# Performance work log

Measured on AMD Instinct MI355X. Metric: run time of the kernel, lower is better.

## Reference

```python
import jax, jax.numpy as jnp
import numpy as np

CTX_WIN = 3  # config.ctx_win_size


def setup_inputs() -> dict:
    key = jax.random.key(0)
    k1, k2, k3 = jax.random.split(key, 3)
    bsz, seq_len, h1, A = 32, 2048, 128, 8
    batch_docIn = jax.random.normal(k1, (bsz, seq_len, h1), dtype=jnp.float32)
    mask = jnp.ones((bsz, seq_len), dtype=bool)
    # params initialized uniform(-0.01, 0.01) as in the torch module
    aspEmbed_weight = jax.random.uniform(k2, (A, CTX_WIN * h1), minval=-0.01, maxval=0.01, dtype=jnp.float32)
    aspProj = jax.random.uniform(k3, (A, h1, h1), minval=-0.01, maxval=0.01, dtype=jnp.float32)
    return {"batch_docIn": batch_docIn, "mask": mask,
            "aspEmbed_weight": aspEmbed_weight, "aspProj": aspProj}


def reference(batch_docIn, mask, aspEmbed_weight, aspProj):
    b, s, h = batch_docIn.shape
    A = aspProj.shape[0]
    win = CTX_WIN
    pad = (win - 1) // 2

    # all aspects at once: [b, A, s, h]
    proj = jnp.einsum('bsd,adh->bash', batch_docIn, aspProj)
    padded = jnp.pad(proj, ((0, 0), (0, 0), (pad, pad), (0, 0)))

    embedR = aspEmbed_weight.reshape(A, h, win)
    # scores[b,a,s] = sum_{d,w} window[b,a,s,d,w] * embedR[a,d,w]
    # computed as a sum over the (small, fixed) window offsets to avoid
    scores = sum(jnp.einsum('bash,ah->bas', padded[:, :, w:w + s, :], embedR[:, :, w])
                 for w in range(win))

    # mask (bool [b,s]) -> masked_fill(~mask, -inf); softmax over seq dim
    scores = jnp.where(mask[:, None, :], scores, -jnp.inf)
    attn = jax.nn.softmax(scores, axis=-1)  # [b, A, s]

    # weighted sum over sequence: [b, A, h]
    rep = jnp.einsum('bash,bas->bah', proj, attn)

    # torch returns attn as [b, A, s] (after transpose/cat) and rep [b, A, h]
    return attn, rep
```

## Files before the change

### kernel.cpp

```cpp
#include <hip/hip_runtime.h>
#include <math.h>

#define BB 32
#define SS 2048
#define HH 128
#define AA 8

typedef _Float16 h2 __attribute__((ext_vector_type(2)));
typedef _Float16 h8 __attribute__((ext_vector_type(8)));
typedef _Float16 f16x8 __attribute__((ext_vector_type(8)));
typedef float f32x4 __attribute__((ext_vector_type(4)));


__global__ __launch_bounds__(128) void prep_kernel(const float* __restrict__ embed,
                                                   const float* __restrict__ proj,
                                                   uint4* __restrict__ bfrag) {
    __shared__ float ua[HH][3];
    int a = blockIdx.x;
    int d = threadIdx.x;
    const float* P = proj + ((size_t)a * HH + d) * HH;
    const float* E = embed + a * (3 * HH);
    float a0 = 0.f, a1 = 0.f, a2 = 0.f;
    for (int h = 0; h < HH; ++h) {
        float x = P[h];
        a0 += x * E[h * 3 + 0];
        a1 += x * E[h * 3 + 1];
        a2 += x * E[h * 3 + 2];
    }
    ua[d][0] = a0; ua[d][1] = a1; ua[d][2] = a2;
    __syncthreads();

    for (int i = d; i < 96; i += 128) {
        int kk = i >> 3, e = i & 7;
        f16x8 v = {0, 0, 0, 0, 0, 0, 0, 0};
        int lane;
        if (e < 4) {
            int q = e;
            lane = q * 16 + a;
            #pragma unroll
            for (int j = 0; j < 8; ++j) {
                int k = kk * 32 + q * 8 + j;
                int w = k >> 7, dd = k & 127;
                v[j] = (_Float16)ua[dd][w];
            }
        } else {
            lane = (e - 4) * 16 + a + 8;
        }
        bfrag[kk * 64 + lane] = __builtin_bit_cast(uint4, v);
    }
}

__global__ __launch_bounds__(256, 4) void tile_kernel(const float* __restrict__ doc,
                                                      const int* __restrict__ mask,
                                                      const uint4* __restrict__ bfrag,
                                                      float* __restrict__ E,
                                                      float* __restrict__ Zpart,
                                                      float* __restrict__ pools) {
    __shared__ __align__(16) unsigned char smraw[21312];
    h2*    dt    = (h2*)smraw;
    float* etile = (float*)(smraw + 19008);
    float* zred  = (float*)(smraw + 19008 + 2048);

    int t = threadIdx.x;
    int lane = t & 63, wave = t >> 6;
    int tile = blockIdx.x;
    int b = blockIdx.y;
    int s0 = tile * 64;

    for (int idx = t; idx < 66 * 16; idx += 256) {
        int row = idx >> 4, c = idx & 15;
        int srow = s0 - 1 + row;
        h8 hv = {0, 0, 0, 0, 0, 0, 0, 0};
        if (srow >= 0 && srow < SS) {
            const float4* src = (const float4*)(doc + ((size_t)b * SS + srow) * HH + c * 8);
            float4 v0 = src[0], v1 = src[1];
            hv[0] = (_Float16)v0.x; hv[1] = (_Float16)v0.y;
            hv[2] = (_Float16)v0.z; hv[3] = (_Float16)v0.w;
            hv[4] = (_Float16)v1.x; hv[5] = (_Float16)v1.y;
            hv[6] = (_Float16)v1.z; hv[7] = (_Float16)v1.w;
        }
        *(h8*)(dt + row * 72 + c * 4) = hv;
    }

    f16x8 bf[12];
    #pragma unroll
    for (int kk = 0; kk < 12; ++kk)
        bf[kk] = __builtin_bit_cast(f16x8, bfrag[kk * 64 + lane]);
    __syncthreads();

    f32x4 acc = {0.f, 0.f, 0.f, 0.f};
    #pragma unroll
    for (int kk = 0; kk < 12; ++kk) {
        int w = kk >> 2;
        int row = wave * 16 + (lane & 15) + w;
        int colh2 = (kk & 3) * 16 + (lane >> 4) * 4;
        f16x8 af = *(const f16x8*)(dt + row * 72 + colh2);
        acc = __builtin_amdgcn_mfma_f32_16x16x32_f16(af, bf[kk], acc, 0, 0, 0);
    }

    const int* mrow = mask + (size_t)b * SS + s0;
    {
        int a = lane & 15;
        int rbase = wave * 16 + (lane >> 4) * 4;
        if (a < 8) {
            float4 ev;
            float* evp = (float*)&ev;
            #pragma unroll
            for (int jj = 0; jj < 4; ++jj) {
                int sl2 = rbase + jj;
                float e = mrow[sl2] ? __expf(acc[jj]) : 0.f;
                evp[jj] = e;
                etile[sl2 * 8 + a] = e;
            }
            *(float4*)(E + ((size_t)(b * AA + a)) * SS + s0 + rbase) = ev;
        }
    }
    __syncthreads();
    if (t < 64) {
        int a = t & 7, g = t >> 3;
        float p = 0.f;
        #pragma unroll
        for (int k = 0; k < 8; ++k) p += etile[(g * 8 + k) * 8 + a];
        zred[g * 8 + a] = p;
    }
    __syncthreads();
    if (t < 8) {
        float z = 0.f;
        #pragma unroll
        for (int g = 0; g < 8; ++g) z += zred[g * 8 + t];
        Zpart[((size_t)(b * AA + t)) * 32 + tile] = z;
    }

    int dq = t & 31, sub = t >> 5;
    float4 pacc[8];
    #pragma unroll
    for (int a = 0; a < 8; ++a) pacc[a] = make_float4(0.f, 0.f, 0.f, 0.f);
    for (int i = 0; i < 8; ++i) {
        int row = 1 + sub * 8 + i;
        uint2 X = *(const uint2*)(dt + row * 72 + dq * 2);
        h2 lo = __builtin_bit_cast(h2, X.x), hi = __builtin_bit_cast(h2, X.y);
        float x0 = (float)lo[0], x1 = (float)lo[1];
        float x2 = (float)hi[0], x3 = (float)hi[1];
        #pragma unroll
        for (int a = 0; a < 8; ++a) {
            float w = etile[(sub * 8 + i) * 8 + a];
            pacc[a].x += w * x0; pacc[a].y += w * x1;
            pacc[a].z += w * x2; pacc[a].w += w * x3;
        }
    }
    #pragma unroll
    for (int a = 0; a < 8; ++a) {
        pacc[a].x += __shfl_xor(pacc[a].x, 32);
        pacc[a].y += __shfl_xor(pacc[a].y, 32);
        pacc[a].z += __shfl_xor(pacc[a].z, 32);
        pacc[a].w += __shfl_xor(pacc[a].w, 32);
    }
    __syncthreads();
    float* cs2 = (float*)smraw;
    if ((t & 63) < 32) {
        #pragma unroll
        for (int a = 0; a < 8; ++a)
            *(float4*)(cs2 + (wave * 8 + a) * 128 + dq * 4) = pacc[a];
    }
    __syncthreads();
    for (int oi = t; oi < 1024; oi += 256) {
        int a = oi >> 7, d = oi & 127;
        float v = (cs2[(0 * 8 + a) * 128 + d] + cs2[(1 * 8 + a) * 128 + d]) +
                  (cs2[(2 * 8 + a) * 128 + d] + cs2[(3 * 8 + a) * 128 + d]);
        pools[(((size_t)(b * 32 + tile)) * AA + a) * HH + d] = v;
    }
}

__global__ __launch_bounds__(256) void finalize_kernel(const float* __restrict__ E,
                                                       const float* __restrict__ Zpart,
                                                       const float* __restrict__ pools,
                                                       const float* __restrict__ proj,
                                                       float* __restrict__ attn,
                                                       float* __restrict__ rep) {
    __shared__ float zbuf[256];
    __shared__ float invZ[8];
    __shared__ float ctxp[2][128];
    __shared__ float ctx[128];
    __shared__ float seg[8][32];
    int t = threadIdx.x;
    int ck = blockIdx.x;
    int b = blockIdx.y;
    int a_rep = ck & 7, hq = ck >> 3;

    zbuf[t] = Zpart[((size_t)(b * AA + (t >> 5))) * 32 + (t & 31)];
    __syncthreads();
    if (t < 8) {
        float z = 0.f;
        #pragma unroll
        for (int k = 0; k < 32; ++k) z += zbuf[t * 32 + k];
        invZ[t] = 1.0f / z;
    }
    __syncthreads();

    for (int oi = t; oi < 512; oi += 256) {
        int a = oi >> 6, s = oi & 63;
        size_t idx = ((size_t)(b * AA + a)) * SS + ck * 64 + s;
        attn[idx] = E[idx] * invZ[a];
    }

    {
        int d = t & 127, half = t >> 7;
        float v = 0.f;
        for (int c = half * 16; c < half * 16 + 16; ++c)
            v += pools[(((size_t)(b * 32 + c)) * AA + a_rep) * HH + d];
        ctxp[half][d] = v;
    }
    __syncthreads();
    if (t < 128) ctx[t] = (ctxp[0][t] + ctxp[1][t]) * invZ[a_rep];
    __syncthreads();

    {
        int h = hq * 32 + (t & 31), sg = t >> 5;
        float v = 0.f;
        for (int d = sg * 16; d < sg * 16 + 16; ++d)
            v += ctx[d] * proj[((size_t)a_rep * HH + d) * HH + h];
        seg[sg][t & 31] = v;
    }
    __syncthreads();
    if (t < 32) {
        float v = 0.f;
        #pragma unroll
        for (int sg = 0; sg < 8; ++sg) v += seg[sg][t];
        rep[((size_t)(b * AA + a_rep)) * HH + hq * 32 + t] = v;
    }
}

extern "C" void kernel_launch(void* const* d_in, const int* in_sizes, int n_in,
                              void* d_out, int out_size, void* d_ws, size_t ws_size,
                              hipStream_t stream) {
    const float* doc   = (const float*)d_in[0];
    const int*   mask  = (const int*)d_in[1];
    const float* embed = (const float*)d_in[2];
    const float* proj  = (const float*)d_in[3];

    float* out  = (float*)d_out;
    float* attn = out;
    float* rep  = out + (size_t)BB * AA * SS;

    uint4* bfrag = (uint4*)d_ws;
    float* E     = (float*)d_ws + 4096;
    float* Zp    = E + (size_t)BB * AA * SS;
    float* pools = Zp + (size_t)BB * AA * 32;

    prep_kernel<<<8, 128, 0, stream>>>(embed, proj, bfrag);
    tile_kernel<<<dim3(32, 32), 256, 0, stream>>>(doc, mask, bfrag, E, Zp, pools);
    finalize_kernel<<<dim3(32, 32), 256, 0, stream>>>(E, Zp, pools, proj, attn, rep);
}
```

Baseline: 28.97 us.

## Compute per-tile attention pooling with MFMA from register-held exp scores

Result: faster. 27.29 us, median of 2 (-5.8%).

```diff
diff --git a/kernel.cpp b/kernel.cpp
--- a/kernel.cpp
+++ b/kernel.cpp
@@ -9,6 +9,7 @@
 typedef _Float16 h2 __attribute__((ext_vector_type(2)));
 typedef _Float16 h8 __attribute__((ext_vector_type(8)));
 typedef _Float16 f16x8 __attribute__((ext_vector_type(8)));
+typedef _Float16 f16x4 __attribute__((ext_vector_type(4)));
 typedef float f32x4 __attribute__((ext_vector_type(4)));
 
 
@@ -56,10 +57,9 @@
                                                       float* __restrict__ E,
                                                       float* __restrict__ Zpart,
                                                       float* __restrict__ pools) {
-    __shared__ __align__(16) unsigned char smraw[21312];
+    __shared__ __align__(16) unsigned char smraw[19264];
     h2*    dt    = (h2*)smraw;
-    float* etile = (float*)(smraw + 19008);
-    float* zred  = (float*)(smraw + 19008 + 2048);
+    float* zredN = (float*)(smraw + 19008);
 
     int t = threadIdx.x;
     int lane = t & 63, wave = t >> 6;
@@ -99,75 +99,63 @@
     }
 
     const int* mrow = mask + (size_t)b * SS + s0;
-    {
-        int a = lane & 15;
-        int rbase = wave * 16 + (lane >> 4) * 4;
-        if (a < 8) {
-            float4 ev;
-            float* evp = (float*)&ev;
+    int a = lane & 15;
+    int rbase = wave * 16 + (lane >> 4) * 4;
+    f16x4 af4;
+    float4 ev;
+    float* evp = (float*)&ev;
+    float zsum = 0.f;
+    #pragma unroll
+    for (int jj = 0; jj < 4; ++jj) {
+        int sl2 = rbase + jj;
+        float e = (a < 8 && mrow[sl2]) ? __expf(acc[jj]) : 0.f;
+        evp[jj] = e;
+        af4[jj] = (_Float16)e;
+        zsum += e;
+    }
+    if (a < 8)
+        *(float4*)(E + ((size_t)(b * AA + a)) * SS + s0 + rbase) = ev;
+    zsum += __shfl_xor(zsum, 16);
+    zsum += __shfl_xor(zsum, 32);
+    if (lane < 16) zredN[wave * 16 + lane] = zsum;
+
+    const _Float16* dtf = (const _Float16*)dt;
+    f32x4 pc[8];
+    #pragma unroll
+    for (int i = 0; i < 8; ++i) pc[i] = (f32x4){0.f, 0.f, 0.f, 0.f};
+    int srow0 = 1 + rbase;
+    #pragma unroll
+    for (int dtile = 0; dtile < 8; ++dtile) {
+        f16x4 bfp;
+        #pragma unroll
+        for (int j = 0; j < 4; ++j)
+            bfp[j] = dtf[(srow0 + j) * 144 + dtile * 16 + a];
+        pc[dtile] = __builtin_amdgcn_mfma_f32_16x16x16f16(af4, bfp, pc[dtile], 0, 0, 0);
+    }
+    __syncthreads();
+
+    float* cs2 = (float*)smraw;
+    if ((lane >> 4) < 2) {
+        int ab = (lane >> 4) * 4;
+        #pragma unroll
+        for (int dtile = 0; dtile < 8; ++dtile) {
+            int d = dtile * 16 + a;
             #pragma unroll
-            for (int jj = 0; jj < 4; ++jj) {
-                int sl2 = rbase + jj;
-                float e = mrow[sl2] ? __expf(acc[jj]) : 0.f;
-                evp[jj] = e;
-                etile[sl2 * 8 + a] = e;
-            }
-            *(float4*)(E + ((size_t)(b * AA + a)) * SS + s0 + rbase) = ev;
+            for (int r = 0; r < 4; ++r)
+                cs2[wave * 1024 + (ab + r) * 128 + d] = pc[dtile][r];
         }
     }
-    __syncthreads();
-    if (t < 64) {
-        int a = t & 7, g = t >> 3;
-        float p = 0.f;
-        #pragma unroll
-        for (int k = 0; k < 8; ++k) p += etile[(g * 8 + k) * 8 + a];
-        zred[g * 8 + a] = p;
-    }
-    __syncthreads();
     if (t < 8) {
-        float z = 0.f;
-        #pragma unroll
-        for (int g = 0; g < 8; ++g) z += zred[g * 8 + t];
+        float z = (zredN[0 * 16 + t] + zredN[1 * 16 + t]) +
+                  (zredN[2 * 16 + t] + zredN[3 * 16 + t]);
         Zpart[((size_t)(b * AA + t)) * 32 + tile] = z;
     }
-
-    int dq = t & 31, sub = t >> 5;
-    float4 pacc[8];
-    #pragma unroll
-    for (int a = 0; a < 8; ++a) pacc[a] = make_float4(0.f, 0.f, 0.f, 0.f);
-    for (int i = 0; i < 8; ++i) {
-        int row = 1 + sub * 8 + i;
-        uint2 X = *(const uint2*)(dt + row * 72 + dq * 2);
-        h2 lo = __builtin_bit_cast(h2, X.x), hi = __builtin_bit_cast(h2, X.y);
-        float x0 = (float)lo[0], x1 = (float)lo[1];
-        float x2 = (float)hi[0], x3 = (float)hi[1];
-        #pragma unroll
-        for (int a = 0; a < 8; ++a) {
-            float w = etile[(sub * 8 + i) * 8 + a];
-            pacc[a].x += w * x0; pacc[a].y += w * x1;
-            pacc[a].z += w * x2; pacc[a].w += w * x3;
-        }
-    }
-    #pragma unroll
-    for (int a = 0; a < 8; ++a) {
-        pacc[a].x += __shfl_xor(pacc[a].x, 32);
-        pacc[a].y += __shfl_xor(pacc[a].y, 32);
-        pacc[a].z += __shfl_xor(pacc[a].z, 32);
-        pacc[a].w += __shfl_xor(pacc[a].w, 32);
-    }
-    __syncthreads();
-    float* cs2 = (float*)smraw;
-    if ((t & 63) < 32) {
-        #pragma unroll
-        for (int a = 0; a < 8; ++a)
-            *(float4*)(cs2 + (wave * 8 + a) * 128 + dq * 4) = pacc[a];
-    }
     __syncthreads();
     for (int oi = t; oi < 1024; oi += 256) {
-        int a = oi >> 7, d = oi & 127;
-        float v = (cs2[(0 * 8 + a) * 128 + d] + cs2[(1 * 8 + a) * 128 + d]) +
-                  (cs2[(2 * 8 + a) * 128 + d] + cs2[(3 * 8 + a) * 128 + d]);
-        pools[(((size_t)(b * 32 + tile)) * AA + a) * HH + d] = v;
+        int aa = oi >> 7, d = oi & 127;
+        float v = (cs2[0 * 1024 + aa * 128 + d] + cs2[1 * 1024 + aa * 128 + d]) +
+                  (cs2[2 * 1024 + aa * 128 + d] + cs2[3 * 1024 + aa * 128 + d]);
+        pools[(((size_t)(b * 32 + tile)) * AA + aa) * HH + d] = v;
     }
 }
 
```
